# Kernel tuning notes

Measured on AMD Instinct MI355X. Metric: run time of the kernel, lower is better.

Reference implementation:

```python
import jax, jax.numpy as jnp
import numpy as np

K, N, E, D = 4, 2048, 4096, 128
BETA = 0.6
EPS = 0.01           # epsilon in hard-sigmoid gating
LAM = 0.05           # lambda_schedule
TC0, TCMAX = 0.3, 0.7
COS_EPS = 1e-8       # F.cosine_similarity eps
MAX_SCORED_EDGES = 500
EDGE_DENSITY = 0.008


def setup_inputs() -> dict:
    key = jax.random.key(0)
    ks = jax.random.split(key, 8)
    s = 0.02
    H = (jax.random.uniform(ks[0], (K, N, E)) < EDGE_DENSITY).astype(jnp.float32)
    X = jax.random.normal(ks[1], (N, D), jnp.float32)
    return dict(
        H=H, X=X, epoch=50,
        mlp_w1=jax.random.normal(ks[2], (K, D, D), jnp.float32) * s,
        mlp_b1=jnp.zeros((K, D), jnp.float32),
        mlp_w2=jax.random.normal(ks[3], (K, D, D), jnp.float32) * s,
        mlp_b2=jnp.zeros((K, D), jnp.float32),
        comp_W=jax.random.normal(ks[4], (K, D, D), jnp.float32) * 0.01,
        att_w1=jax.random.normal(ks[5], (K, D, D // 2), jnp.float32) * s,
        att_b1=jnp.zeros((K, D // 2), jnp.float32),
        att_w2=jax.random.normal(ks[6], (K, D // 2, 1), jnp.float32) * s,
        att_b2=jnp.zeros((K, 1), jnp.float32),
    )


def reference(H, X, epoch, mlp_w1, mlp_b1, mlp_w2, mlp_b2, comp_W,
              att_w1, att_b1, att_w2, att_b2):
    # ---- component level (Eq. 4, batched over K) ----
    h1 = jax.nn.relu(jnp.einsum('nd,kdh->knh', X, mlp_w1) + mlp_b1[:, None, :])
    Xk = jnp.einsum('knh,khe->kne', h1, mlp_w2) + mlp_b2[:, None, :]        # [K,N,D]
    a1 = jax.nn.relu(jnp.einsum('knd,kdh->knh', Xk, att_w1) + att_b1[:, None, :])
    att = jax.nn.sigmoid(jnp.einsum('knh,kho->kno', a1, att_w2) + att_b2[:, None, :])
    S_att = att.mean(axis=(1, 2))                                            # [K]
    frob = jnp.sqrt((comp_W ** 2).sum(axis=(1, 2)))                          # ||W_k||_F
    featn = jnp.sqrt((Xk ** 2).sum(axis=(1, 2)))                             # ||MLP(X_k)||_2 (Frobenius)
    imp = BETA * frob * featn + (1.0 - BETA) * S_att
    pi_c = jax.nn.softmax(imp)
    theta_c = TC0 + (1.0 - jnp.exp(-LAM * epoch)) * (TCMAX - TC0)            # Eq. 3 schedule
    gates = jnp.clip((pi_c - theta_c) / EPS + 0.5, 0.0, 1.0)                 # hard sigmoid
    # K_min = max(1, int(0.1*K)) = 1 -> force top-1 gate open
    keep = jax.nn.one_hot(jnp.argmax(gates), K, dtype=gates.dtype)
    gates = jnp.maximum(gates, keep)

    xnorm = jnp.linalg.norm(X, axis=1)                                       # [N]
    xhat = X / jnp.maximum(xnorm, COS_EPS)[:, None]
    er = jnp.arange(E)
    eye = jnp.eye(N, dtype=bool)

    Hp_l, eg_l, npi_l = [], [], []
    for k in range(K):  # small fixed component count
        Hk = H[k]
        mask = Hk > 0                                                        # [N,E]
        cnt = mask.sum(axis=0)                                               # nodes per hyperedge
        order = jnp.cumsum(mask, axis=0)
        i = jnp.argmax(mask, axis=0)                                         # first incident node
        j = jnp.argmax(mask & (order == 2), axis=0)                          # second incident node
        cos = (xhat[i] * xhat[j]).sum(-1)                                    # [E]
        A = Hk[i, er] * Hk[j, er]                                            # A_ij per edge
        # torch loop: only first 500 edges scored; <2-node edges get 0.1; rest 0
        imp_e = jnp.where(er < MAX_SCORED_EDGES,
                          jnp.where(cnt >= 2, A * cos, 0.1), 0.0)
        pi_e = jax.nn.softmax(imp_e)
        theta_e = jnp.minimum(theta_c, pi_e.mean() + jnp.std(pi_e, ddof=1))  # torch.std unbiased
        eg = jnp.clip((pi_e - theta_e) / EPS + 0.5, 0.0, 1.0)
        eg = jnp.where((eg.sum() < 1.0) & (er == jnp.argmax(pi_e)), 1.0, eg)
        eg_eff = jnp.where(gates[k] > 0.5, eg, jnp.ones_like(eg))
        Hp = Hk * gates[k] * eg_eff[None, :]                                 # pruned incidence

        # ---- node level (Eq. 7) on pruned graph ----
        B = (Hp > 0).astype(Hk.dtype)
        Adj = ((B @ B.T) > 0) & (~eye)                                       # shared-hyperedge neighbors
        degf = Adj.sum(axis=1).astype(Hk.dtype)
        nsum = Adj.astype(Hk.dtype) @ xhat                                   # sum of neighbor unit vecs
        avg = jnp.where(degf > 0, (xhat * nsum).sum(-1) / jnp.maximum(degf, 1.0), 0.0)
        npi = jax.nn.softmax(avg * xnorm)
        Hp_l.append(Hp); eg_l.append(eg); npi_l.append(npi)

    return (jnp.stack(Hp_l), gates, jnp.stack(eg_l), jnp.stack(npi_l))
```

## Files before the change

kernel.cpp:

```cpp
#include <hip/hip_runtime.h>
#include <math.h>

#define KCOMP 4
#define NN 2048
#define EE 4096
#define DD 128
#define MAXNE 96
#define MAXSE 500
#define BETA_C 0.6f
#define EPS_G 0.01f
#define LAM_S 0.05f
#define TC0_C 0.3f
#define TCMAX_C 0.7f
#define COS_EPS_C 1e-8f

typedef float vf4 __attribute__((ext_vector_type(4)));

static const size_t OFF_XHAT   = 0;
static const size_t OFF_XNORM  = 1048576;
static const size_t OFF_SCAL   = 1056768;
static const size_t OFF_NCNT   = 1057024;
static const size_t OFF_EMASK  = 1089792;
static const size_t OFF_NELIST = 5284096;
static const size_t OFF_IMPE   = 6856960;
static const size_t OFF_EGS    = 6865152;
static const size_t OFF_Z      = 6930688;
static const size_t OFF_FEAT   = 6963456;
static const size_t OFF_ATT    = 6965504;
static const size_t OFF_FROB   = 6967552;

__global__ __launch_bounds__(1024) void k_d1(
    const float4* __restrict__ H4, unsigned* __restrict__ emask,
    const float* __restrict__ X, float* __restrict__ xhat, float* __restrict__ xnorm,
    const float* __restrict__ w1, const float* __restrict__ b1,
    const float* __restrict__ w2, const float* __restrict__ b2,
    const float* __restrict__ aw1, const float* __restrict__ ab1,
    const float* __restrict__ aw2, const float* __restrict__ ab2,
    const float4* __restrict__ compW4, int* __restrict__ ncnt,
    float* __restrict__ featA, float* __restrict__ attA, float* __restrict__ frobA) {
  __shared__ float smem[16416];
  int b = blockIdx.x, t = threadIdx.x;
  if (b < 128) {
    int k = b >> 5;
    int bx = b & 31;
    float* Xs  = smem;
    float* H1s = smem + 8192;
    float* A1s = H1s;
    float* red = smem + 16384;
    int n0 = bx * 64;
    for (int i = t; i < 64 * 128; i += 1024) Xs[i] = X[(size_t)n0 * 128 + i];
    __syncthreads();

    int h = t & 127, g = t >> 7;
    const float* W1 = w1 + (size_t)k * 128 * 128;
    float acc[8];
    {
      float bb = b1[k * 128 + h];
#pragma unroll
      for (int rr = 0; rr < 8; ++rr) acc[rr] = bb;
    }
    for (int d = 0; d < 128; d += 4) {
      float wa = W1[(d + 0) * 128 + h];
      float wb = W1[(d + 1) * 128 + h];
      float wc = W1[(d + 2) * 128 + h];
      float wd2 = W1[(d + 3) * 128 + h];
#pragma unroll
      for (int rr = 0; rr < 8; ++rr) {
        float4 x = *(const float4*)&Xs[(g * 8 + rr) * 128 + d];
        acc[rr] = fmaf(x.x, wa, acc[rr]); acc[rr] = fmaf(x.y, wb, acc[rr]);
        acc[rr] = fmaf(x.z, wc, acc[rr]); acc[rr] = fmaf(x.w, wd2, acc[rr]);
      }
    }
#pragma unroll
    for (int rr = 0; rr < 8; ++rr) H1s[(g * 8 + rr) * 128 + h] = fmaxf(acc[rr], 0.f);
    __syncthreads();

    const float* W2 = w2 + (size_t)k * 128 * 128;
    {
      float bb = b2[k * 128 + h];
#pragma unroll
      for (int rr = 0; rr < 8; ++rr) acc[rr] = bb;
    }
    for (int d = 0; d < 128; d += 4) {
      float wa = W2[(d + 0) * 128 + h];
      float wb = W2[(d + 1) * 128 + h];
      float wc = W2[(d + 2) * 128 + h];
      float wd2 = W2[(d + 3) * 128 + h];
#pragma unroll
      for (int rr = 0; rr < 8; ++rr) {
        float4 x = *(const float4*)&H1s[(g * 8 + rr) * 128 + d];
        acc[rr] = fmaf(x.x, wa, acc[rr]); acc[rr] = fmaf(x.y, wb, acc[rr]);
        acc[rr] = fmaf(x.z, wc, acc[rr]); acc[rr] = fmaf(x.w, wd2, acc[rr]);
      }
    }
    float fpart = 0.f;
    __syncthreads();
#pragma unroll
    for (int rr = 0; rr < 8; ++rr) {
      Xs[(g * 8 + rr) * 128 + h] = acc[rr];
      fpart = fmaf(acc[rr], acc[rr], fpart);
    }
    __syncthreads();

    int h2 = t & 63, g4 = t >> 6;
    const float* AW1 = aw1 + (size_t)k * 128 * 64;
    float a4[4];
    {
      float ab = ab1[k * 64 + h2];
#pragma unroll
      for (int q = 0; q < 4; ++q) a4[q] = ab;
    }
    for (int d = 0; d < 128; d += 4) {
      float wa = AW1[(d + 0) * 64 + h2];
      float wb = AW1[(d + 1) * 64 + h2];
      float wc = AW1[(d + 2) * 64 + h2];
      float wd2 = AW1[(d + 3) * 64 + h2];
#pragma unroll
      for (int q = 0; q < 4; ++q) {
        float4 x = *(const float4*)&Xs[(g4 * 4 + q) * 128 + d];
        a4[q] = fmaf(x.x, wa, a4[q]); a4[q] = fmaf(x.y, wb, a4[q]);
        a4[q] = fmaf(x.z, wc, a4[q]); a4[q] = fmaf(x.w, wd2, a4[q]);
      }
    }
    __syncthreads();
#pragma unroll
    for (int q = 0; q < 4; ++q) A1s[(g4 * 4 + q) * 64 + h2] = fmaxf(a4[q], 0.f);
    __syncthreads();

    float attsum = 0.f;
    if (t < 64) {
      const float* AW2 = aw2 + (size_t)k * 64;
      float a = ab2[k];
      for (int d = 0; d < 64; d += 4) {
        float4 av = *(const float4*)&A1s[t * 64 + d];
        a = fmaf(av.x, AW2[d + 0], a);
        a = fmaf(av.y, AW2[d + 1], a);
        a = fmaf(av.z, AW2[d + 2], a);
        a = fmaf(av.w, AW2[d + 3], a);
      }
      attsum = 1.f / (1.f + expf(-a));
    }
    for (int o = 32; o > 0; o >>= 1) {
      fpart  += __shfl_xor(fpart, o, 64);
      attsum += __shfl_xor(attsum, o, 64);
    }
    int wv = t >> 6, ln = t & 63;
    if (ln == 0) { red[wv] = fpart; red[16 + wv] = attsum; }
    __syncthreads();
    if (t == 0) {
      float fs = 0.f, as = 0.f;
#pragma unroll
      for (int i = 0; i < 16; i++) { fs += red[i]; as += red[16 + i]; }
      featA[k * 128 + bx] = fs;
      attA[k * 128 + bx]  = as;
    }
    return;
  }
  if (b < 384) {
    unsigned* lds = (unsigned*)smem;
    int sb = b - 128;
    int k = sb >> 6;
    int rem = sb & 63;
    int ch_super = rem >> 4;
    int e4_super = rem & 15;
    int chi = t >> 6;
    int e4i = t & 63;
    int ch = ch_super * 16 + chi;
    int e4 = e4_super * 64 + e4i;
    int n0 = ch * 32;
    const float4* p = H4 + ((size_t)(k * NN + n0)) * (EE / 4) + e4;
    unsigned w0 = 0, w1b = 0, w2b = 0, w3 = 0;
    for (int rb = 0; rb < 32; rb += 8) {
      float4 v[8];
#pragma unroll
      for (int u = 0; u < 8; ++u) v[u] = p[(size_t)(rb + u) * (EE / 4)];
#pragma unroll
      for (int u = 0; u < 8; ++u) {
        unsigned bit = 1u << (rb + u);
        w0  |= (v[u].x > 0.f) ? bit : 0u;
        w1b |= (v[u].y > 0.f) ? bit : 0u;
        w2b |= (v[u].z > 0.f) ? bit : 0u;
        w3  |= (v[u].w > 0.f) ? bit : 0u;
      }
    }
    int el = e4i * 4;
    lds[(el + 0) * 17 + chi] = w0;
    lds[(el + 1) * 17 + chi] = w1b;
    lds[(el + 2) * 17 + chi] = w2b;
    lds[(el + 3) * 17 + chi] = w3;
    __syncthreads();
    int e_base = e4_super * 256;
    int wi = t & 15;
    int eo = t >> 4;
#pragma unroll
    for (int it = 0; it < 4; ++it) {
      int e_local = it * 64 + eo;
      emask[((size_t)(k * EE) + e_base + e_local) * 64 + ch_super * 16 + wi] =
          lds[e_local * 17 + wi];
    }
    return;
  }
  if (b < 512) {
    int xb = b - 384;
    if (t < 64) ncnt[xb * 64 + t] = 0;
    int node = xb * 16 + (t >> 6);
    int lane = t & 63;
    float2 v = ((const float2*)X)[(size_t)node * 64 + lane];
    float ss = v.x * v.x + v.y * v.y;
    for (int o = 32; o > 0; o >>= 1) ss += __shfl_xor(ss, o, 64);
    float nrm = sqrtf(ss);
    float den = fmaxf(nrm, COS_EPS_C);
    if (lane == 0) xnorm[node] = nrm;
    float2 o2; o2.x = v.x / den; o2.y = v.y / den;
    ((float2*)xhat)[(size_t)node * 64 + lane] = o2;
    return;
  }
  {
    int fb = b - 512;
    int k = fb >> 2, idx = fb & 3;
    float* red = smem;
    float4 v = compW4[(size_t)k * 4096 + idx * 1024 + t];
    float s = v.x * v.x + v.y * v.y + v.z * v.z + v.w * v.w;
    for (int o = 32; o > 0; o >>= 1) s += __shfl_xor(s, o, 64);
    int wv = t >> 6, ln = t & 63;
    if (ln == 0) red[wv] = s;
    __syncthreads();
    if (t == 0) {
      float fs = 0.f;
#pragma unroll
      for (int i = 0; i < 16; i++) fs += red[i];
      frobA[k * 4 + idx] = fs;
    }
  }
}

__global__ void k_d2(const unsigned* __restrict__ emask, int* __restrict__ ncnt,
                     unsigned short* __restrict__ nelist, const float* __restrict__ xhat,
                     float* __restrict__ impE) {
  int t = threadIdx.x;
  int k = blockIdx.y;
  int bx = blockIdx.x;
  if (bx < 16) {
    const unsigned* base = emask + (size_t)k * EE * 64 + (size_t)bx * 256 * 64;
    int e0 = bx * 256;
    for (int i = t; i < 256 * 64; i += 256) {
      unsigned wdw = base[i];
      if (!wdw) continue;
      int e = e0 + (i >> 6);
      int wrd = i & 63;
      do {
        int bit = __builtin_ctz(wdw); wdw &= wdw - 1;
        int node = wrd * 32 + bit;
        int slot = atomicAdd(&ncnt[k * NN + node], 1);
        if (slot < MAXNE)
          nelist[((size_t)(k * NN + node)) * MAXNE + slot] = (unsigned short)e;
      } while (wdw);
    }
    return;
  }
  int e = (bx - 16) * 4 + (t >> 6);
  int lane = t & 63;
  unsigned w = emask[((size_t)(k * EE) + e) * 64 + lane];
  int pc = __popc(w);
  for (int o = 32; o > 0; o >>= 1) pc += __shfl_xor(pc, o, 64);
  float impv = 0.1f;
  if (pc >= 2) {
    unsigned l1 = w ? (unsigned)((lane << 5) + __builtin_ctz(w)) : 0xffffffffu;
    unsigned wr = w & (w - 1);
    unsigned l2 = wr ? (unsigned)((lane << 5) + __builtin_ctz(wr)) : 0xffffffffu;
    unsigned g1 = l1;
    for (int o = 32; o > 0; o >>= 1) {
      unsigned x = (unsigned)__shfl_xor((int)g1, o, 64);
      g1 = g1 < x ? g1 : x;
    }
    unsigned cand = (l1 == g1) ? l2 : l1;
    unsigned g2 = cand;
    for (int o = 32; o > 0; o >>= 1) {
      unsigned x = (unsigned)__shfl_xor((int)g2, o, 64);
      g2 = g2 < x ? g2 : x;
    }
    float2 xi = ((const float2*)xhat)[(size_t)g1 * 64 + lane];
    float2 xj = ((const float2*)xhat)[(size_t)g2 * 64 + lane];
    float d = xi.x * xj.x + xi.y * xj.y;
    for (int o = 32; o > 0; o >>= 1) d += __shfl_xor(d, o, 64);
    impv = d;
  }
  if (lane == 0) impE[k * 512 + e] = impv;
}

__device__ __forceinline__ float blockReduceSum16(float v, float* red, int t) {
  for (int o = 32; o > 0; o >>= 1) v += __shfl_xor(v, o, 64);
  __syncthreads();
  if ((t & 63) == 0) red[t >> 6] = v;
  __syncthreads();
  float s = red[0];
#pragma unroll
  for (int i = 1; i < 16; i++) s += red[i];
  return s;
}

__global__ void k_edgegate(const float* __restrict__ impE,
                           const float* __restrict__ featA, const float* __restrict__ attA,
                           const float* __restrict__ frobA, float* __restrict__ scal,
                           const int* __restrict__ epoch, float* __restrict__ out_gates,
                           float* __restrict__ egscaled, float* __restrict__ out_eg) {
  __shared__ float red[16];
  __shared__ int redi[16];
  __shared__ float imps[KCOMP];
  int k = blockIdx.x;
  int t = threadIdx.x;
  int wv0 = t >> 6, ln0 = t & 63;
  if (wv0 < KCOMP) {
    float pf = (ln0 < 32) ? featA[wv0 * 128 + ln0] : 0.f;
    float pa = (ln0 < 32) ? attA[wv0 * 128 + ln0] : 0.f;
    float pr = (ln0 < 4) ? frobA[wv0 * 4 + ln0] : 0.f;
    for (int o = 32; o > 0; o >>= 1) {
      pf += __shfl_xor(pf, o, 64);
      pa += __shfl_xor(pa, o, 64);
      pr += __shfl_xor(pr, o, 64);
    }
    if (ln0 == 0)
      imps[wv0] = BETA_C * sqrtf(pr) * sqrtf(pf) + (1.f - BETA_C) * (pa / (float)NN);
  }
  __syncthreads();
  float gates[KCOMP];
  float tc;
  {
    float mx = imps[0];
    for (int kk = 1; kk < KCOMP; kk++) mx = fmaxf(mx, imps[kk]);
    float ex[KCOMP], ssum = 0.f;
    for (int kk = 0; kk < KCOMP; kk++) { ex[kk] = expf(imps[kk] - mx); ssum += ex[kk]; }
    tc = TC0_C + (1.f - expf(-LAM_S * (float)epoch[0])) * (TCMAX_C - TC0_C);
    for (int kk = 0; kk < KCOMP; kk++) {
      float pi = ex[kk] / ssum;
      gates[kk] = fminf(fmaxf((pi - tc) / EPS_G + 0.5f, 0.f), 1.f);
    }
    int am = 0; float bv2 = gates[0];
    for (int kk = 1; kk < KCOMP; kk++) if (gates[kk] > bv2) { bv2 = gates[kk]; am = kk; }
    gates[am] = fmaxf(gates[am], 1.f);
  }
  if (t == 0) {
    scal[12 + k] = gates[k];
    if (k == 0) for (int kk = 0; kk < KCOMP; kk++) out_gates[kk] = gates[kk];
  }
  float imp[4];
#pragma unroll
  for (int j = 0; j < 4; j++) {
    int e = t + j * 1024;
    imp[j] = (e < MAXSE) ? impE[k * 512 + e] : 0.f;
  }
  float m = fmaxf(fmaxf(imp[0], imp[1]), fmaxf(imp[2], imp[3]));
  for (int o = 32; o > 0; o >>= 1) m = fmaxf(m, __shfl_xor(m, o, 64));
  __syncthreads();
  if ((t & 63) == 0) red[t >> 6] = m;
  __syncthreads();
  m = red[0];
#pragma unroll
  for (int i = 1; i < 16; i++) m = fmaxf(m, red[i]);
  float p[4], psum = 0.f;
#pragma unroll
  for (int j = 0; j < 4; j++) { p[j] = expf(imp[j] - m); psum += p[j]; }
  float S = blockReduceSum16(psum, red, t);
  float pi[4], tot = 0.f;
#pragma unroll
  for (int j = 0; j < 4; j++) { pi[j] = p[j] / S; tot += pi[j]; }
  float T = blockReduceSum16(tot, red, t);
  float mean = T / (float)EE;
  float devs = 0.f;
#pragma unroll
  for (int j = 0; j < 4; j++) { float d = pi[j] - mean; devs = fmaf(d, d, devs); }
  float V = blockReduceSum16(devs, red, t);
  float stdv = sqrtf(V / (float)(EE - 1));
  float theta = fminf(tc, mean + stdv);
  float eg[4], egsum = 0.f;
#pragma unroll
  for (int j = 0; j < 4; j++) {
    eg[j] = fminf(fmaxf((pi[j] - theta) / EPS_G + 0.5f, 0.f), 1.f);
    egsum += eg[j];
  }
  float EGS = blockReduceSum16(egsum, red, t);
  float bv = -1e30f; int bi = 0x7fffffff;
#pragma unroll
  for (int j = 0; j < 4; j++) if (pi[j] > bv) { bv = pi[j]; bi = t + j * 1024; }
  for (int o = 32; o > 0; o >>= 1) {
    float ov = __shfl_xor(bv, o, 64); int oi = __shfl_xor(bi, o, 64);
    if (ov > bv || (ov == bv && oi < bi)) { bv = ov; bi = oi; }
  }
  __syncthreads();
  if ((t & 63) == 0) { red[t >> 6] = bv; redi[t >> 6] = bi; }
  __syncthreads();
  float abv = red[0]; int abi = redi[0];
#pragma unroll
  for (int i = 1; i < 16; i++) {
    float ov = red[i]; int oi = redi[i];
    if (ov > abv || (ov == abv && oi < abi)) { abv = ov; abi = oi; }
  }
  float g = gates[k];
#pragma unroll
  for (int j = 0; j < 4; j++) {
    int e = t + j * 1024;
    float egv = eg[j];
    if (EGS < 1.f && e == abi) egv = 1.f;
    out_eg[(size_t)k * EE + e] = egv;
    float eff = (g > 0.5f) ? egv : 1.f;
    egscaled[k * EE + e] = g * eff;
  }
}

__global__ void k_hprow(const unsigned* __restrict__ emask,
                        const int* __restrict__ ncnt, const unsigned short* __restrict__ nelist,
                        const float* __restrict__ egs, const float* __restrict__ scal,
                        const float* __restrict__ xhat, const float* __restrict__ xnorm,
                        float* __restrict__ out, float* __restrict__ z) {
  __shared__ float row[EE];
  __shared__ unsigned short elds[MAXNE];
  __shared__ unsigned wpart[4][64];
  __shared__ unsigned short list[2048];
  __shared__ int cnt_s;
  __shared__ float sred[4];
  int k = blockIdx.y, n = blockIdx.x, t = threadIdx.x;
  float g = scal[12 + k];
  vf4* o4 = (vf4*)(out + ((size_t)(k * NN + n)) * EE);
  if (g <= 0.f) {
    vf4 z4 = {0.f, 0.f, 0.f, 0.f};
#pragma unroll
    for (int i = 0; i < 4; i++) __builtin_nontemporal_store(z4, &o4[t + i * 256]);
    if (t == 0) z[k * NN + n] = 0.f;
    return;
  }
  int ec = ncnt[k * NN + n]; if (ec > MAXNE) ec = MAXNE;
  if (t < ec) elds[t] = nelist[((size_t)(k * NN + n)) * MAXNE + t];
  vf4* row4 = (vf4*)row;
  vf4 z4 = {0.f, 0.f, 0.f, 0.f};
#pragma unroll
  for (int i = 0; i < 4; i++) row4[t + i * 256] = z4;
  if (t == 0) cnt_s = 0;
  __syncthreads();
  if (t < ec) {
    int e = elds[t];
    row[e] = egs[k * EE + e];
  }
  __syncthreads();
#pragma unroll
  for (int i = 0; i < 4; i++) __builtin_nontemporal_store(row4[t + i * 256], &o4[t + i * 256]);
  int lane = t & 63, wv = t >> 6;
  unsigned acc = 0;
  for (int it = wv; it < ec; it += 4) {
    int e = (int)elds[it];
    if (row[e] > 0.f) acc |= emask[((size_t)(k * EE) + e) * 64 + lane];
  }
  wpart[wv][lane] = acc;
  __syncthreads();
  if (t < 64) {
    unsigned w = wpart[0][t] | wpart[1][t] | wpart[2][t] | wpart[3][t];
    if (t == (n >> 5)) w &= ~(1u << (n & 31));
    int c = __popc(w);
    if (c > 0) {
      int base = atomicAdd(&cnt_s, c);
      while (w) {
        int b = __builtin_ctz(w); w &= w - 1;
        list[base++] = (unsigned short)((t << 5) + b);
      }
    }
  }
  __syncthreads();
  int cnt = cnt_s;
  if (cnt == 0) { if (t == 0) z[k * NN + n] = 0.f; return; }
  int fc = lane & 31, hh = lane >> 5;
  float4 xn4 = ((const float4*)xhat)[(size_t)n * 32 + fc];
  float a = 0.f;
#pragma unroll 4
  for (int it = wv * 2 + hh; it < cnt; it += 8) {
    int m = (int)list[it];
    float4 xm = ((const float4*)xhat)[(size_t)m * 32 + fc];
    a += xn4.x * xm.x + xn4.y * xm.y + xn4.z * xm.z + xn4.w * xm.w;
  }
  for (int o = 32; o > 0; o >>= 1) a += __shfl_xor(a, o, 64);
  if (lane == 0) sred[wv] = a;
  __syncthreads();
  if (t == 0) {
    float s = sred[0] + sred[1] + sred[2] + sred[3];
    z[k * NN + n] = (s / (float)cnt) * xnorm[n];
  }
}

__global__ void k_npi(const float* __restrict__ z, float* __restrict__ out_npi) {
  __shared__ float red[4];
  int k = blockIdx.x, t = threadIdx.x;
  float v[8]; float m = -1e30f;
#pragma unroll
  for (int j = 0; j < 8; j++) { v[j] = z[k * NN + t + j * 256]; m = fmaxf(m, v[j]); }
  for (int o = 32; o > 0; o >>= 1) m = fmaxf(m, __shfl_xor(m, o, 64));
  if ((t & 63) == 0) red[t >> 6] = m;
  __syncthreads();
  m = fmaxf(fmaxf(red[0], red[1]), fmaxf(red[2], red[3]));
  __syncthreads();
  float pe[8]; float s = 0.f;
#pragma unroll
  for (int j = 0; j < 8; j++) { pe[j] = expf(v[j] - m); s += pe[j]; }
  for (int o = 32; o > 0; o >>= 1) s += __shfl_xor(s, o, 64);
  if ((t & 63) == 0) red[t >> 6] = s;
  __syncthreads();
  s = red[0] + red[1] + red[2] + red[3];
#pragma unroll
  for (int j = 0; j < 8; j++) out_npi[k * NN + t + j * 256] = pe[j] / s;
}

extern "C" void kernel_launch(void* const* d_in, const int* in_sizes, int n_in,
                              void* d_out, int out_size, void* d_ws, size_t ws_size,
                              hipStream_t stream) {
  const float* H     = (const float*)d_in[0];
  const float* X     = (const float*)d_in[1];
  const int*   epoch = (const int*)d_in[2];
  const float* w1    = (const float*)d_in[3];
  const float* b1    = (const float*)d_in[4];
  const float* w2    = (const float*)d_in[5];
  const float* b2    = (const float*)d_in[6];
  const float* compW = (const float*)d_in[7];
  const float* aw1   = (const float*)d_in[8];
  const float* ab1   = (const float*)d_in[9];
  const float* aw2   = (const float*)d_in[10];
  const float* ab2   = (const float*)d_in[11];

  char* ws = (char*)d_ws;
  float* xhat  = (float*)(ws + OFF_XHAT);
  float* xnorm = (float*)(ws + OFF_XNORM);
  float* scal  = (float*)(ws + OFF_SCAL);
  int*   ncnt  = (int*)(ws + OFF_NCNT);
  unsigned* emask = (unsigned*)(ws + OFF_EMASK);
  unsigned short* nelist = (unsigned short*)(ws + OFF_NELIST);
  float* impE  = (float*)(ws + OFF_IMPE);
  float* egs   = (float*)(ws + OFF_EGS);
  float* zbuf  = (float*)(ws + OFF_Z);
  float* featA = (float*)(ws + OFF_FEAT);
  float* attA  = (float*)(ws + OFF_ATT);
  float* frobA = (float*)(ws + OFF_FROB);

  float* out       = (float*)d_out;
  float* out_gates = out + (size_t)KCOMP * NN * EE;
  float* out_eg    = out_gates + KCOMP;
  float* out_npi   = out_eg + (size_t)KCOMP * EE;

  k_d1<<<528, 1024, 0, stream>>>((const float4*)H, emask, X, xhat, xnorm,
                                 w1, b1, w2, b2, aw1, ab1, aw2, ab2,
                                 (const float4*)compW, ncnt, featA, attA, frobA);
  k_d2<<<dim3(141, KCOMP), 256, 0, stream>>>(emask, ncnt, nelist, xhat, impE);
  k_edgegate<<<KCOMP, 1024, 0, stream>>>(impE, featA, attA, frobA, scal, epoch,
                                         out_gates, egs, out_eg);
  k_hprow<<<dim3(NN, KCOMP), 256, 0, stream>>>(emask, ncnt, nelist, egs, scal, xhat, xnorm,
                                               out, zbuf);
  k_npi<<<KCOMP, 256, 0, stream>>>(zbuf, out_npi);
}
```

Baseline: 372.5 us.

## Build node-to-edge lists inside bitmask kernel and drop separate scatter pass

The per-node hyperedge list construction (atomic slot allocation plus nelist write) moves from k_d2 into k_d1, where each thread already holds the freshly computed 32-node bitmask words. This removes the 16 extra blocks per component in k_d2 that re-read the whole emask to scatter edges. Because ncnt is now incremented in k_d1, its zeroing moves to a hipMemsetAsync before the launch. The atomics now run inside the heavy H-scanning blocks, and the order of entries within each node's list changes, which could alter downstream results if order matters.

```diff
diff --git a/kernel.cpp b/kernel.cpp
--- a/kernel.cpp
+++ b/kernel.cpp
@@ -37,6 +37,7 @@
     const float* __restrict__ aw1, const float* __restrict__ ab1,
     const float* __restrict__ aw2, const float* __restrict__ ab2,
     const float4* __restrict__ compW4, int* __restrict__ ncnt,
+    unsigned short* __restrict__ nelist,
     float* __restrict__ featA, float* __restrict__ attA, float* __restrict__ frobA) {
   __shared__ float smem[16416];
   int b = blockIdx.x, t = threadIdx.x;
@@ -188,6 +189,22 @@
     lds[(el + 1) * 17 + chi] = w1b;
     lds[(el + 2) * 17 + chi] = w2b;
     lds[(el + 3) * 17 + chi] = w3;
+    {
+      int ebase = e4 * 4;
+      unsigned ws[4] = {w0, w1b, w2b, w3};
+#pragma unroll
+      for (int j = 0; j < 4; ++j) {
+        unsigned wd = ws[j];
+        while (wd) {
+          int bit = __builtin_ctz(wd); wd &= wd - 1;
+          int node = n0 + bit;
+          int slot = atomicAdd(&ncnt[k * NN + node], 1);
+          if (slot < MAXNE)
+            nelist[((size_t)(k * NN + node)) * MAXNE + slot] =
+                (unsigned short)(ebase + j);
+        }
+      }
+    }
     __syncthreads();
     int e_base = e4_super * 256;
     int wi = t & 15;
@@ -202,7 +219,6 @@
   }
   if (b < 512) {
     int xb = b - 384;
-    if (t < 64) ncnt[xb * 64 + t] = 0;
     int node = xb * 16 + (t >> 6);
     int lane = t & 63;
     float2 v = ((const float2*)X)[(size_t)node * 64 + lane];
@@ -234,31 +250,12 @@
   }
 }
 
-__global__ void k_d2(const unsigned* __restrict__ emask, int* __restrict__ ncnt,
-                     unsigned short* __restrict__ nelist, const float* __restrict__ xhat,
+__global__ void k_d2(const unsigned* __restrict__ emask, const float* __restrict__ xhat,
                      float* __restrict__ impE) {
   int t = threadIdx.x;
   int k = blockIdx.y;
   int bx = blockIdx.x;
-  if (bx < 16) {
-    const unsigned* base = emask + (size_t)k * EE * 64 + (size_t)bx * 256 * 64;
-    int e0 = bx * 256;
-    for (int i = t; i < 256 * 64; i += 256) {
-      unsigned wdw = base[i];
-      if (!wdw) continue;
-      int e = e0 + (i >> 6);
-      int wrd = i & 63;
-      do {
-        int bit = __builtin_ctz(wdw); wdw &= wdw - 1;
-        int node = wrd * 32 + bit;
-        int slot = atomicAdd(&ncnt[k * NN + node], 1);
-        if (slot < MAXNE)
-          nelist[((size_t)(k * NN + node)) * MAXNE + slot] = (unsigned short)e;
-      } while (wdw);
-    }
-    return;
-  }
-  int e = (bx - 16) * 4 + (t >> 6);
+  int e = bx * 4 + (t >> 6);
   int lane = t & 63;
   unsigned w = emask[((size_t)(k * EE) + e) * 64 + lane];
   int pc = __popc(w);
@@ -541,10 +538,11 @@
   float* out_eg    = out_gates + KCOMP;
   float* out_npi   = out_eg + (size_t)KCOMP * EE;
 
+  hipMemsetAsync(ncnt, 0, (size_t)KCOMP * NN * sizeof(int), stream);
   k_d1<<<528, 1024, 0, stream>>>((const float4*)H, emask, X, xhat, xnorm,
                                  w1, b1, w2, b2, aw1, ab1, aw2, ab2,
-                                 (const float4*)compW, ncnt, featA, attA, frobA);
-  k_d2<<<dim3(141, KCOMP), 256, 0, stream>>>(emask, ncnt, nelist, xhat, impE);
+                                 (const float4*)compW, ncnt, nelist, featA, attA, frobA);
+  k_d2<<<dim3(125, KCOMP), 256, 0, stream>>>(emask, xhat, impE);
   k_edgegate<<<KCOMP, 1024, 0, stream>>>(impE, featA, attA, frobA, scal, epoch,
                                          out_gates, egs, out_eg);
   k_hprow<<<dim3(NN, KCOMP), 256, 0, stream>>>(emask, ncnt, nelist, egs, scal, xhat, xnorm,
```

Result: faster. 301.2 us (-19.2%).
